# Kernel tuning notes

Hardware: AMD Instinct MI355X
Metric: run time of the kernel (lower is better)

Reference implementation:

```python
import jax, jax.numpy as jnp
import numpy as np

B, T, F, D, H = 16, 512, 32, 256, 256
EPS = 1e-5


def _layernorm(y, g, b):
    m = jnp.mean(y, axis=-1, keepdims=True)
    v = jnp.mean((y - m) ** 2, axis=-1, keepdims=True)
    return (y - m) / jnp.sqrt(v + EPS) * g + b


def setup_inputs() -> dict:
    key = jax.random.key(0)
    ks = jax.random.split(key, 24)
    s = lambda fan_in: 1.0 / np.sqrt(fan_in)
    u = lambda k, shape, fan_in: jax.random.uniform(k, shape, jnp.float32, -s(fan_in), s(fan_in))
    return {
        "x": jax.random.normal(ks[0], (B, T, F), jnp.float32),
        # per-feature Linear(1, D), stacked over F
        "proj_w": u(ks[1], (F, D), 1),
        "proj_b": u(ks[2], (F, D), 1),
        # per-feature scorer GRN(D, H, 1), stacked over F
        "sc_fc1_w": u(ks[3], (F, H, D), D),
        "sc_fc1_b": u(ks[4], (F, H), D),
        "sc_fc2_w": u(ks[5], (F, 1, H), H),
        "sc_fc2_b": u(ks[6], (F, 1), H),
        "sc_gate_w": u(ks[7], (F, 1, 1), 1),
        "sc_gate_b": u(ks[8], (F, 1), 1),
        "sc_skip_w": u(ks[9], (F, 1, D), D),
        "sc_skip_b": u(ks[10], (F, 1), D),
        "sc_ln_g": jnp.ones((F, 1), jnp.float32),
        "sc_ln_b": jnp.zeros((F, 1), jnp.float32),
        # post GRN(D, H, D); in_dim == out_dim -> skip is identity
        "post_fc1_w": u(ks[11], (H, D), D),
        "post_fc1_b": u(ks[12], (H,), D),
        "post_fc2_w": u(ks[13], (D, H), H),
        "post_fc2_b": u(ks[14], (D,), H),
        "post_gate_w": u(ks[15], (D, D), D),
        "post_gate_b": u(ks[16], (D,), D),
        "post_ln_g": jnp.ones((D,), jnp.float32),
        "post_ln_b": jnp.zeros((D,), jnp.float32),
    }


def reference(x, proj_w, proj_b, sc_fc1_w, sc_fc1_b, sc_fc2_w, sc_fc2_b,
              sc_gate_w, sc_gate_b, sc_skip_w, sc_skip_b, sc_ln_g, sc_ln_b,
              post_fc1_w, post_fc1_b, post_fc2_w, post_fc2_b,
              post_gate_w, post_gate_b, post_ln_g, post_ln_b):
    # per-feature embedding: Linear(1 -> D), batched over F
    # E: [B, T, F, D]
    E = x[..., None] * proj_w[None, None] + proj_b[None, None]

    # per-feature scorer GRN(D, H, 1), all F at once
    h = jax.nn.elu(jnp.einsum("btfd,fhd->btfh", E, sc_fc1_w) + sc_fc1_b)
    h = jnp.einsum("btfh,foh->btfo", h, sc_fc2_w) + sc_fc2_b  # [B,T,F,1]
    g = jax.nn.sigmoid(jnp.einsum("btfo,fpo->btfp", h, sc_gate_w) + sc_gate_b)
    skip = jnp.einsum("btfd,fod->btfo", E, sc_skip_w) + sc_skip_b
    y = g * h + (1.0 - g) * skip
    S = _layernorm(y, sc_ln_g, sc_ln_b)  # [B,T,F,1] (last dim size 1)

    # softmax over features, weighted mixture
    W = jax.nn.softmax(S, axis=2)
    mix = jnp.sum(E * W, axis=2)  # [B,T,D]

    # post GRN(D, H, D), skip = identity
    h2 = jax.nn.elu(mix @ post_fc1_w.T + post_fc1_b)
    h2 = h2 @ post_fc2_w.T + post_fc2_b
    g2 = jax.nn.sigmoid(h2 @ post_gate_w.T + post_gate_b)
    y2 = g2 * h2 + (1.0 - g2) * mix
    return _layernorm(y2, post_ln_g, post_ln_b)
```

## Files before the change

### kernel.cpp

```cpp
#include <hip/hip_runtime.h>
#include <hip/hip_bf16.h>
#include <math.h>


typedef __bf16 bf16;
typedef __bf16 bf16x8 __attribute__((ext_vector_type(8)));
typedef __bf16 bf16x4 __attribute__((ext_vector_type(4)));
typedef float f32x4 __attribute__((ext_vector_type(4)));

#define NTOK 8192
#define D_   256
#define F_   32

#define OFF_C      512
#define OFF_WPROJT 2048
#define OFF_FC1    32768
#define OFF_FC2    163840
#define OFF_GATE   294912


__global__ __launch_bounds__(256) void vsn_prep(
    const float* __restrict__ proj_w, const float* __restrict__ proj_b,
    const float* __restrict__ sc_ln_b,
    const float* __restrict__ w1, const float* __restrict__ w2,
    const float* __restrict__ w3,
    float* __restrict__ wsC, bf16* __restrict__ wsWT,
    bf16* __restrict__ o1, bf16* __restrict__ o2, bf16* __restrict__ o3)
{
  const int blk = blockIdx.x;
  if (blk < 24) {
    int g = blk * 256 + threadIdx.x;
    int m = g >> 11;
    int c = g & 2047;
    const float* src = (m == 0) ? w1 : (m == 1) ? w2 : w3;
    bf16* dst = (m == 0) ? o1 : (m == 1) ? o2 : o3;
    int row = c >> 3, ks = c & 7;
    int j = row >> 4, lm = row & 15;
    const float* sp = src + row * 256 + ks * 32;
    bf16* dp = dst + j * 4096 + ks * 512 + lm * 32;
    #pragma unroll
    for (int q = 0; q < 4; q++) {
      float4 a = ((const float4*)sp)[2 * q];
      float4 b = ((const float4*)sp)[2 * q + 1];
      bf16x8 v = {(bf16)a.x, (bf16)a.y, (bf16)a.z, (bf16)a.w,
                  (bf16)b.x, (bf16)b.y, (bf16)b.z, (bf16)b.w};
      *(bf16x8*)(dp + q * 8) = v;
    }
  } else {
    const int d = threadIdx.x;
    float wv[F_];
    float mx = -3.0e38f;
    #pragma unroll
    for (int f = 0; f < F_; f++) { wv[f] = sc_ln_b[f]; mx = fmaxf(mx, wv[f]); }
    float se = 0.0f;
    #pragma unroll
    for (int f = 0; f < F_; f++) { wv[f] = __expf(wv[f] - mx); se += wv[f]; }
    float inv = 1.0f / se;
    float acc = 0.0f;
    #pragma unroll
    for (int f = 0; f < F_; f++) {
      float wf = wv[f] * inv;
      acc += wf * proj_b[f * D_ + d];
      wsWT[d * F_ + f] = (bf16)(wf * proj_w[f * D_ + d]);
    }
    wsC[d] = acc;
  }
}

__global__ __launch_bounds__(256, 2) void vsn_main(
    const float* __restrict__ x,
    const float* __restrict__ wsC,
    const bf16* __restrict__ WT,
    const bf16* __restrict__ FC1, const float* __restrict__ fc1_b,
    const bf16* __restrict__ FC2, const float* __restrict__ fc2_b,
    const bf16* __restrict__ GATE, const float* __restrict__ gate_b,
    const float* __restrict__ ln_g, const float* __restrict__ ln_b,
    float* __restrict__ out)
{
  __shared__ bf16  sAct[2][16][264];
  __shared__ float sLN[4][16][2];

  const int tid  = threadIdx.x;
  const int w    = tid >> 6;
  const int lane = tid & 63;
  const int lm   = lane & 15;
  const int lq   = lane >> 4;
  const int j0   = w * 4;
  const int tok0 = blockIdx.x * 16;

  bf16x4 mixh[4];
  {
    const float* xp = x + (size_t)(tok0 + lm) * F_ + lq * 8;
    float4 x0 = *(const float4*)xp;
    float4 x1 = *(const float4*)(xp + 4);
    bf16x8 a0 = {(bf16)x0.x, (bf16)x0.y, (bf16)x0.z, (bf16)x0.w,
                 (bf16)x1.x, (bf16)x1.y, (bf16)x1.z, (bf16)x1.w};
    #pragma unroll
    for (int jj = 0; jj < 4; jj++) {
      int n = (j0 + jj) * 16 + lm;
      bf16x8 b = *(const bf16x8*)(WT + n * F_ + lq * 8);
      float cv = wsC[n];
      f32x4 acc = {cv, cv, cv, cv};
      acc = __builtin_amdgcn_mfma_f32_16x16x32_bf16(a0, b, acc, 0, 0, 0);
      bf16x4 mh = {(bf16)acc[0], (bf16)acc[1], (bf16)acc[2], (bf16)acc[3]};
      mixh[jj] = mh;
      #pragma unroll
      for (int r = 0; r < 4; r++) sAct[0][lq * 4 + r][n] = mh[r];
    }
  }
  __syncthreads();

  auto gemmPhase = [&](int src, const bf16* __restrict__ W, f32x4* acc) {
    bf16x8 af[8];
    #pragma unroll
    for (int ks = 0; ks < 8; ks++)
      af[ks] = *(const bf16x8*)(&sAct[src][lm][ks * 32 + lq * 8]);
    const bf16* base = W + j0 * 4096 + lm * 32 + lq * 8;
    bf16x8 bb[8];
    #pragma unroll
    for (int ks = 0; ks < 8; ks++)
      bb[ks] = *(const bf16x8*)(base + ks * 512);
    #pragma unroll
    for (int jj = 0; jj < 4; jj++) {
      bf16x8 bn[8];
      if (jj < 3) {
        const bf16* nb = base + (jj + 1) * 4096;
        #pragma unroll
        for (int ks = 0; ks < 8; ks++)
          bn[ks] = *(const bf16x8*)(nb + ks * 512);
      }
      f32x4 a = {0.f, 0.f, 0.f, 0.f};
      acc[jj] = a;
      #pragma unroll
      for (int ks = 0; ks < 8; ks++)
        acc[jj] = __builtin_amdgcn_mfma_f32_16x16x32_bf16(af[ks], bb[ks], acc[jj], 0, 0, 0);
      if (jj < 3) {
        #pragma unroll
        for (int ks = 0; ks < 8; ks++) bb[ks] = bn[ks];
      }
    }
  };

  {
    f32x4 acc[4];
    gemmPhase(0, FC1, acc);
    #pragma unroll
    for (int jj = 0; jj < 4; jj++) {
      int n = (j0 + jj) * 16 + lm;
      float bias = fc1_b[n];
      #pragma unroll
      for (int r = 0; r < 4; r++) {
        float v = acc[jj][r] + bias;
        v = (v > 0.0f) ? v : (__expf(v) - 1.0f);
        sAct[1][lq * 4 + r][n] = (bf16)v;
      }
    }
  }
  __syncthreads();

  bf16x4 h2h[4];
  {
    f32x4 acc[4];
    gemmPhase(1, FC2, acc);
    #pragma unroll
    for (int jj = 0; jj < 4; jj++) {
      int n = (j0 + jj) * 16 + lm;
      float bias = fc2_b[n];
      bf16x4 hh;
      #pragma unroll
      for (int r = 0; r < 4; r++) {
        hh[r] = (bf16)(acc[jj][r] + bias);
        sAct[0][lq * 4 + r][n] = hh[r];
      }
      h2h[jj] = hh;
    }
  }
  __syncthreads();

  f32x4 acc4[4];
  gemmPhase(0, GATE, acc4);
  float rs[4] = {0.f, 0.f, 0.f, 0.f}, rq[4] = {0.f, 0.f, 0.f, 0.f};
  #pragma unroll
  for (int jj = 0; jj < 4; jj++) {
    int n = (j0 + jj) * 16 + lm;
    float bias = gate_b[n];
    #pragma unroll
    for (int r = 0; r < 4; r++) {
      float s = acc4[jj][r] + bias;
      float g = 1.0f / (1.0f + __expf(-s));
      float y = g * (float)h2h[jj][r] + (1.0f - g) * (float)mixh[jj][r];
      acc4[jj][r] = y;
      rs[r] += y;
      rq[r] += y * y;
    }
  }

  #pragma unroll
  for (int r = 0; r < 4; r++) {
    #pragma unroll
    for (int off = 1; off < 16; off <<= 1) {
      rs[r] += __shfl_xor(rs[r], off);
      rq[r] += __shfl_xor(rq[r], off);
    }
  }
  if (lm == 0) {
    #pragma unroll
    for (int r = 0; r < 4; r++) {
      sLN[w][lq * 4 + r][0] = rs[r];
      sLN[w][lq * 4 + r][1] = rq[r];
    }
  }
  __syncthreads();

  const float inv_d = 1.0f / 256.0f;
  float mean[4], rstd[4];
  #pragma unroll
  for (int r = 0; r < 4; r++) {
    int row = lq * 4 + r;
    float S = sLN[0][row][0] + sLN[1][row][0] + sLN[2][row][0] + sLN[3][row][0];
    float Q = sLN[0][row][1] + sLN[1][row][1] + sLN[2][row][1] + sLN[3][row][1];
    float m = S * inv_d;
    mean[r] = m;
    rstd[r] = rsqrtf(Q * inv_d - m * m + 1e-5f);
  }
  #pragma unroll
  for (int jj = 0; jj < 4; jj++) {
    int n = (j0 + jj) * 16 + lm;
    float lg = ln_g[n], lb = ln_b[n];
    #pragma unroll
    for (int r = 0; r < 4; r++) {
      float o = (acc4[jj][r] - mean[r]) * rstd[r] * lg + lb;
      out[(size_t)(tok0 + lq * 4 + r) * D_ + n] = o;
    }
  }
}

extern "C" void kernel_launch(void* const* d_in, const int* in_sizes, int n_in,
                              void* d_out, int out_size, void* d_ws, size_t ws_size,
                              hipStream_t stream) {
  (void)in_sizes; (void)n_in; (void)ws_size; (void)out_size;
  const float* x      = (const float*)d_in[0];
  const float* proj_w = (const float*)d_in[1];
  const float* proj_b = (const float*)d_in[2];
  const float* sclnb  = (const float*)d_in[12];
  const float* fc1w   = (const float*)d_in[13];
  const float* fc1b   = (const float*)d_in[14];
  const float* fc2w   = (const float*)d_in[15];
  const float* fc2b   = (const float*)d_in[16];
  const float* gw     = (const float*)d_in[17];
  const float* gb     = (const float*)d_in[18];
  const float* lng    = (const float*)d_in[19];
  const float* lnb    = (const float*)d_in[20];

  char* ws = (char*)d_ws;
  float* wsC   = (float*)(ws + OFF_C);
  bf16*  wsWT  = (bf16*)(ws + OFF_WPROJT);
  bf16*  bFC1  = (bf16*)(ws + OFF_FC1);
  bf16*  bFC2  = (bf16*)(ws + OFF_FC2);
  bf16*  bGATE = (bf16*)(ws + OFF_GATE);

  vsn_prep<<<25, 256, 0, stream>>>(proj_w, proj_b, sclnb, fc1w, fc2w, gw,
                                   wsC, wsWT, bFC1, bFC2, bGATE);
  vsn_main<<<NTOK / 16, 256, 0, stream>>>(x, wsC, wsWT,
                                          bFC1, fc1b, bFC2, fc2b, bGATE, gb,
                                          lng, lnb, (float*)d_out);
}
```

Before: 121.3 us.

## Fold gate weight into fc2 algebraically and process 32 tokens per block

Precomputes Wgate·Wfc2 and the matching folded bias in the prep kernel, so the gate GEMM reads the fc1 activations directly and runs alongside the fc2 GEMM in one phase. This removes one GEMM stage, one LDS round trip and one barrier. Each block also handles 32 tokens instead of 16, so every loaded weight fragment is reused across two MFMA tiles. The costs are a heavier prep kernel (a serial 256×256×256 fp32 product), more registers per thread with occupancy cut to one block per CU, a grid of only 256 blocks, and a change in bf16 rounding from multiplying the weights ahead of time.

```diff
diff --git a/kernel.cpp b/kernel.cpp
--- a/kernel.cpp
+++ b/kernel.cpp
@@ -13,27 +13,29 @@
 #define F_   32
 
 #define OFF_C      512
-#define OFF_WPROJT 2048
+#define OFF_BP     1536
+#define OFF_WPROJT 4096
 #define OFF_FC1    32768
 #define OFF_FC2    163840
-#define OFF_GATE   294912
+#define OFF_GF     294912
 
 
 __global__ __launch_bounds__(256) void vsn_prep(
     const float* __restrict__ proj_w, const float* __restrict__ proj_b,
     const float* __restrict__ sc_ln_b,
-    const float* __restrict__ w1, const float* __restrict__ w2,
-    const float* __restrict__ w3,
-    float* __restrict__ wsC, bf16* __restrict__ wsWT,
-    bf16* __restrict__ o1, bf16* __restrict__ o2, bf16* __restrict__ o3)
+    const float* __restrict__ fc1w, const float* __restrict__ fc2w,
+    const float* __restrict__ fc2b,
+    const float* __restrict__ gatew, const float* __restrict__ gateb,
+    float* __restrict__ wsC, float* __restrict__ wsBp, bf16* __restrict__ wsWT,
+    bf16* __restrict__ oFC1, bf16* __restrict__ oFC2, bf16* __restrict__ oGF)
 {
   const int blk = blockIdx.x;
-  if (blk < 24) {
+  if (blk < 16) {
     int g = blk * 256 + threadIdx.x;
     int m = g >> 11;
     int c = g & 2047;
-    const float* src = (m == 0) ? w1 : (m == 1) ? w2 : w3;
-    bf16* dst = (m == 0) ? o1 : (m == 1) ? o2 : o3;
+    const float* src = (m == 0) ? fc1w : fc2w;
+    bf16* dst = (m == 0) ? oFC1 : oFC2;
     int row = c >> 3, ks = c & 7;
     int j = row >> 4, lm = row & 15;
     const float* sp = src + row * 256 + ks * 32;
@@ -46,7 +48,7 @@
                   (bf16)b.x, (bf16)b.y, (bf16)b.z, (bf16)b.w};
       *(bf16x8*)(dp + q * 8) = v;
     }
-  } else {
+  } else if (blk == 16) {
     const int d = threadIdx.x;
     float wv[F_];
     float mx = -3.0e38f;
@@ -64,21 +66,48 @@
       wsWT[d * F_ + f] = (bf16)(wf * proj_w[f * D_ + d]);
     }
     wsC[d] = acc;
+  } else {
+    __shared__ float gs[4][257];
+    const int rb = (blk - 17) * 4;
+    const int c = threadIdx.x;
+    #pragma unroll
+    for (int r = 0; r < 4; r++) gs[r][c] = gatew[(rb + r) * 256 + c];
+    __syncthreads();
+    float a0 = 0.f, a1 = 0.f, a2 = 0.f, a3 = 0.f;
+    for (int k = 0; k < 256; k++) {
+      float f = fc2w[k * 256 + c];
+      a0 += gs[0][k] * f;
+      a1 += gs[1][k] * f;
+      a2 += gs[2][k] * f;
+      a3 += gs[3][k] * f;
+    }
+    float accr[4] = {a0, a1, a2, a3};
+    #pragma unroll
+    for (int r = 0; r < 4; r++) {
+      int row = rb + r;
+      oGF[(row >> 4) * 4096 + (c >> 5) * 512 + (row & 15) * 32 + (c & 31)] =
+          (bf16)accr[r];
+    }
+    if (c < 4) {
+      float s = gateb[rb + c];
+      for (int k = 0; k < 256; k++) s += gs[c][k] * fc2b[k];
+      wsBp[rb + c] = s;
+    }
   }
 }
 
-__global__ __launch_bounds__(256, 2) void vsn_main(
+__global__ __launch_bounds__(256, 1) void vsn_main(
     const float* __restrict__ x,
     const float* __restrict__ wsC,
     const bf16* __restrict__ WT,
     const bf16* __restrict__ FC1, const float* __restrict__ fc1_b,
     const bf16* __restrict__ FC2, const float* __restrict__ fc2_b,
-    const bf16* __restrict__ GATE, const float* __restrict__ gate_b,
+    const bf16* __restrict__ GF, const float* __restrict__ bprime,
     const float* __restrict__ ln_g, const float* __restrict__ ln_b,
     float* __restrict__ out)
 {
-  __shared__ bf16  sAct[2][16][264];
-  __shared__ float sLN[4][16][2];
+  __shared__ bf16  sAct[2][32][264];
+  __shared__ float sLN[4][32][2];
 
   const int tid  = threadIdx.x;
   const int w    = tid >> 6;
@@ -86,36 +115,46 @@
   const int lm   = lane & 15;
   const int lq   = lane >> 4;
   const int j0   = w * 4;
-  const int tok0 = blockIdx.x * 16;
-
-  bf16x4 mixh[4];
+  const int tok0 = blockIdx.x * 32;
+
+  bf16x4 mixh[2][4];
   {
-    const float* xp = x + (size_t)(tok0 + lm) * F_ + lq * 8;
-    float4 x0 = *(const float4*)xp;
-    float4 x1 = *(const float4*)(xp + 4);
-    bf16x8 a0 = {(bf16)x0.x, (bf16)x0.y, (bf16)x0.z, (bf16)x0.w,
-                 (bf16)x1.x, (bf16)x1.y, (bf16)x1.z, (bf16)x1.w};
+    bf16x8 a[2];
+    #pragma unroll
+    for (int t = 0; t < 2; t++) {
+      const float* xp = x + (size_t)(tok0 + t * 16 + lm) * F_ + lq * 8;
+      float4 x0 = *(const float4*)xp;
+      float4 x1 = *(const float4*)(xp + 4);
+      bf16x8 av = {(bf16)x0.x, (bf16)x0.y, (bf16)x0.z, (bf16)x0.w,
+                   (bf16)x1.x, (bf16)x1.y, (bf16)x1.z, (bf16)x1.w};
+      a[t] = av;
+    }
     #pragma unroll
     for (int jj = 0; jj < 4; jj++) {
       int n = (j0 + jj) * 16 + lm;
       bf16x8 b = *(const bf16x8*)(WT + n * F_ + lq * 8);
       float cv = wsC[n];
-      f32x4 acc = {cv, cv, cv, cv};
-      acc = __builtin_amdgcn_mfma_f32_16x16x32_bf16(a0, b, acc, 0, 0, 0);
-      bf16x4 mh = {(bf16)acc[0], (bf16)acc[1], (bf16)acc[2], (bf16)acc[3]};
-      mixh[jj] = mh;
-      #pragma unroll
-      for (int r = 0; r < 4; r++) sAct[0][lq * 4 + r][n] = mh[r];
+      #pragma unroll
+      for (int t = 0; t < 2; t++) {
+        f32x4 acc = {cv, cv, cv, cv};
+        acc = __builtin_amdgcn_mfma_f32_16x16x32_bf16(a[t], b, acc, 0, 0, 0);
+        bf16x4 mh = {(bf16)acc[0], (bf16)acc[1], (bf16)acc[2], (bf16)acc[3]};
+        mixh[t][jj] = mh;
+        #pragma unroll
+        for (int r = 0; r < 4; r++) sAct[0][t * 16 + lq * 4 + r][n] = mh[r];
+      }
     }
   }
   __syncthreads();
 
-  auto gemmPhase = [&](int src, const bf16* __restrict__ W, f32x4* acc) {
-    bf16x8 af[8];
-    #pragma unroll
-    for (int ks = 0; ks < 8; ks++)
-      af[ks] = *(const bf16x8*)(&sAct[src][lm][ks * 32 + lq * 8]);
-    const bf16* base = W + j0 * 4096 + lm * 32 + lq * 8;
+  {
+    bf16x8 af[2][8];
+    #pragma unroll
+    for (int t = 0; t < 2; t++)
+      #pragma unroll
+      for (int ks = 0; ks < 8; ks++)
+        af[t][ks] = *(const bf16x8*)(&sAct[0][t * 16 + lm][ks * 32 + lq * 8]);
+    const bf16* base = FC1 + j0 * 4096 + lm * 32 + lq * 8;
     bf16x8 bb[8];
     #pragma unroll
     for (int ks = 0; ks < 8; ks++)
@@ -129,108 +168,121 @@
         for (int ks = 0; ks < 8; ks++)
           bn[ks] = *(const bf16x8*)(nb + ks * 512);
       }
-      f32x4 a = {0.f, 0.f, 0.f, 0.f};
-      acc[jj] = a;
-      #pragma unroll
-      for (int ks = 0; ks < 8; ks++)
-        acc[jj] = __builtin_amdgcn_mfma_f32_16x16x32_bf16(af[ks], bb[ks], acc[jj], 0, 0, 0);
+      f32x4 acc0 = {0.f, 0.f, 0.f, 0.f}, acc1 = {0.f, 0.f, 0.f, 0.f};
+      #pragma unroll
+      for (int ks = 0; ks < 8; ks++) {
+        acc0 = __builtin_amdgcn_mfma_f32_16x16x32_bf16(af[0][ks], bb[ks], acc0, 0, 0, 0);
+        acc1 = __builtin_amdgcn_mfma_f32_16x16x32_bf16(af[1][ks], bb[ks], acc1, 0, 0, 0);
+      }
+      int n = (j0 + jj) * 16 + lm;
+      float bias = fc1_b[n];
+      #pragma unroll
+      for (int r = 0; r < 4; r++) {
+        float v0 = acc0[r] + bias;
+        v0 = (v0 > 0.0f) ? v0 : (__expf(v0) - 1.0f);
+        sAct[1][lq * 4 + r][n] = (bf16)v0;
+        float v1 = acc1[r] + bias;
+        v1 = (v1 > 0.0f) ? v1 : (__expf(v1) - 1.0f);
+        sAct[1][16 + lq * 4 + r][n] = (bf16)v1;
+      }
       if (jj < 3) {
         #pragma unroll
         for (int ks = 0; ks < 8; ks++) bb[ks] = bn[ks];
       }
     }
-  };
-
+  }
+  __syncthreads();
+
+  f32x4 y2[2][4];
   {
-    f32x4 acc[4];
-    gemmPhase(0, FC1, acc);
+    bf16x8 af[2][8];
+    #pragma unroll
+    for (int t = 0; t < 2; t++)
+      #pragma unroll
+      for (int ks = 0; ks < 8; ks++)
+        af[t][ks] = *(const bf16x8*)(&sAct[1][t * 16 + lm][ks * 32 + lq * 8]);
+    const bf16* baseF = FC2 + j0 * 4096 + lm * 32 + lq * 8;
+    const bf16* baseG = GF  + j0 * 4096 + lm * 32 + lq * 8;
+    #pragma unroll
+    for (int jj = 0; jj < 4; jj++) {
+      bf16x8 bF[8], bG[8];
+      #pragma unroll
+      for (int ks = 0; ks < 8; ks++) {
+        bF[ks] = *(const bf16x8*)(baseF + jj * 4096 + ks * 512);
+        bG[ks] = *(const bf16x8*)(baseG + jj * 4096 + ks * 512);
+      }
+      f32x4 hF0 = {0.f,0.f,0.f,0.f}, hF1 = {0.f,0.f,0.f,0.f};
+      f32x4 hG0 = {0.f,0.f,0.f,0.f}, hG1 = {0.f,0.f,0.f,0.f};
+      #pragma unroll
+      for (int ks = 0; ks < 8; ks++) {
+        hF0 = __builtin_amdgcn_mfma_f32_16x16x32_bf16(af[0][ks], bF[ks], hF0, 0, 0, 0);
+        hF1 = __builtin_amdgcn_mfma_f32_16x16x32_bf16(af[1][ks], bF[ks], hF1, 0, 0, 0);
+        hG0 = __builtin_amdgcn_mfma_f32_16x16x32_bf16(af[0][ks], bG[ks], hG0, 0, 0, 0);
+        hG1 = __builtin_amdgcn_mfma_f32_16x16x32_bf16(af[1][ks], bG[ks], hG1, 0, 0, 0);
+      }
+      int n = (j0 + jj) * 16 + lm;
+      float b2v = fc2_b[n];
+      float bpv = bprime[n];
+      #pragma unroll
+      for (int r = 0; r < 4; r++) {
+        float h20 = hF0[r] + b2v;
+        float g0  = 1.0f / (1.0f + __expf(-(hG0[r] + bpv)));
+        y2[0][jj][r] = g0 * h20 + (1.0f - g0) * (float)mixh[0][jj][r];
+        float h21 = hF1[r] + b2v;
+        float g1  = 1.0f / (1.0f + __expf(-(hG1[r] + bpv)));
+        y2[1][jj][r] = g1 * h21 + (1.0f - g1) * (float)mixh[1][jj][r];
+      }
+    }
+  }
+
+  #pragma unroll
+  for (int t = 0; t < 2; t++) {
+    float rs[4] = {0.f,0.f,0.f,0.f}, rq[4] = {0.f,0.f,0.f,0.f};
+    #pragma unroll
+    for (int jj = 0; jj < 4; jj++)
+      #pragma unroll
+      for (int r = 0; r < 4; r++) {
+        float y = y2[t][jj][r];
+        rs[r] += y;
+        rq[r] += y * y;
+      }
+    #pragma unroll
+    for (int r = 0; r < 4; r++) {
+      #pragma unroll
+      for (int off = 1; off < 16; off <<= 1) {
+        rs[r] += __shfl_xor(rs[r], off);
+        rq[r] += __shfl_xor(rq[r], off);
+      }
+      if (lm == 0) {
+        sLN[w][t * 16 + lq * 4 + r][0] = rs[r];
+        sLN[w][t * 16 + lq * 4 + r][1] = rq[r];
+      }
+    }
+  }
+  __syncthreads();
+
+  const float inv_d = 1.0f / 256.0f;
+  #pragma unroll
+  for (int t = 0; t < 2; t++) {
+    float mean[4], rstd[4];
+    #pragma unroll
+    for (int r = 0; r < 4; r++) {
+      int row = t * 16 + lq * 4 + r;
+      float S = sLN[0][row][0] + sLN[1][row][0] + sLN[2][row][0] + sLN[3][row][0];
+      float Q = sLN[0][row][1] + sLN[1][row][1] + sLN[2][row][1] + sLN[3][row][1];
+      float m = S * inv_d;
+      mean[r] = m;
+      rstd[r] = rsqrtf(Q * inv_d - m * m + 1e-5f);
+    }
     #pragma unroll
     for (int jj = 0; jj < 4; jj++) {
       int n = (j0 + jj) * 16 + lm;
-      float bias = fc1_b[n];
+      float lg = ln_g[n], lb = ln_b[n];
       #pragma unroll
       for (int r = 0; r < 4; r++) {
-        float v = acc[jj][r] + bias;
-        v = (v > 0.0f) ? v : (__expf(v) - 1.0f);
-        sAct[1][lq * 4 + r][n] = (bf16)v;
-      }
-    }
-  }
-  __syncthreads();
-
-  bf16x4 h2h[4];
-  {
-    f32x4 acc[4];
-    gemmPhase(1, FC2, acc);
-    #pragma unroll
-    for (int jj = 0; jj < 4; jj++) {
-      int n = (j0 + jj) * 16 + lm;
-      float bias = fc2_b[n];
-      bf16x4 hh;
-      #pragma unroll
-      for (int r = 0; r < 4; r++) {
-        hh[r] = (bf16)(acc[jj][r] + bias);
-        sAct[0][lq * 4 + r][n] = hh[r];
-      }
-      h2h[jj] = hh;
-    }
-  }
-  __syncthreads();
-
-  f32x4 acc4[4];
-  gemmPhase(0, GATE, acc4);
-  float rs[4] = {0.f, 0.f, 0.f, 0.f}, rq[4] = {0.f, 0.f, 0.f, 0.f};
-  #pragma unroll
-  for (int jj = 0; jj < 4; jj++) {
-    int n = (j0 + jj) * 16 + lm;
-    float bias = gate_b[n];
-    #pragma unroll
-    for (int r = 0; r < 4; r++) {
-      float s = acc4[jj][r] + bias;
-      float g = 1.0f / (1.0f + __expf(-s));
-      float y = g * (float)h2h[jj][r] + (1.0f - g) * (float)mixh[jj][r];
-      acc4[jj][r] = y;
-      rs[r] += y;
-      rq[r] += y * y;
-    }
-  }
-
-  #pragma unroll
-  for (int r = 0; r < 4; r++) {
-    #pragma unroll
-    for (int off = 1; off < 16; off <<= 1) {
-      rs[r] += __shfl_xor(rs[r], off);
-      rq[r] += __shfl_xor(rq[r], off);
-    }
-  }
-  if (lm == 0) {
-    #pragma unroll
-    for (int r = 0; r < 4; r++) {
-      sLN[w][lq * 4 + r][0] = rs[r];
-      sLN[w][lq * 4 + r][1] = rq[r];
-    }
-  }
-  __syncthreads();
-
-  const float inv_d = 1.0f / 256.0f;
-  float mean[4], rstd[4];
-  #pragma unroll
-  for (int r = 0; r < 4; r++) {
-    int row = lq * 4 + r;
-    float S = sLN[0][row][0] + sLN[1][row][0] + sLN[2][row][0] + sLN[3][row][0];
-    float Q = sLN[0][row][1] + sLN[1][row][1] + sLN[2][row][1] + sLN[3][row][1];
-    float m = S * inv_d;
-    mean[r] = m;
-    rstd[r] = rsqrtf(Q * inv_d - m * m + 1e-5f);
-  }
-  #pragma unroll
-  for (int jj = 0; jj < 4; jj++) {
-    int n = (j0 + jj) * 16 + lm;
-    float lg = ln_g[n], lb = ln_b[n];
-    #pragma unroll
-    for (int r = 0; r < 4; r++) {
-      float o = (acc4[jj][r] - mean[r]) * rstd[r] * lg + lb;
-      out[(size_t)(tok0 + lq * 4 + r) * D_ + n] = o;
+        float o = (y2[t][jj][r] - mean[r]) * rstd[r] * lg + lb;
+        out[(size_t)(tok0 + t * 16 + lq * 4 + r) * D_ + n] = o;
+      }
     }
   }
 }
@@ -254,14 +306,15 @@
 
   char* ws = (char*)d_ws;
   float* wsC   = (float*)(ws + OFF_C);
+  float* wsBp  = (float*)(ws + OFF_BP);
   bf16*  wsWT  = (bf16*)(ws + OFF_WPROJT);
   bf16*  bFC1  = (bf16*)(ws + OFF_FC1);
   bf16*  bFC2  = (bf16*)(ws + OFF_FC2);
-  bf16*  bGATE = (bf16*)(ws + OFF_GATE);
-
-  vsn_prep<<<25, 256, 0, stream>>>(proj_w, proj_b, sclnb, fc1w, fc2w, gw,
-                                   wsC, wsWT, bFC1, bFC2, bGATE);
-  vsn_main<<<NTOK / 16, 256, 0, stream>>>(x, wsC, wsWT,
-                                          bFC1, fc1b, bFC2, fc2b, bGATE, gb,
+  bf16*  bGF   = (bf16*)(ws + OFF_GF);
+
+  vsn_prep<<<81, 256, 0, stream>>>(proj_w, proj_b, sclnb, fc1w, fc2w, fc2b,
+                                   gw, gb, wsC, wsBp, wsWT, bFC1, bFC2, bGF);
+  vsn_main<<<NTOK / 32, 256, 0, stream>>>(x, wsC, wsWT,
+                                          bFC1, fc1b, bFC2, fc2b, bGF, wsBp,
                                           lng, lnb, (float*)d_out);
 }
```

After: 130.4 us. 1.07x slower.

## Process 32 tokens per block with 8 waves, reusing weight fragments

Applied to the files above, without the earlier changes.

Each block now handles 32 tokens with 512 threads (8 waves), and each wave computes 2 output column tiles for two 16-token row tiles instead of 4 tiles for one. Each B-weight fragment loaded from global memory now feeds two MFMAs, which halves weight traffic per token and gives more independent MFMA chains. The cost is a grid of only 256 blocks, which may underfill a GPU with 256 CUs, plus larger LDS usage and more register pressure per wave.

```diff
diff --git a/kernel.cpp b/kernel.cpp
--- a/kernel.cpp
+++ b/kernel.cpp
@@ -67,7 +67,7 @@
   }
 }
 
-__global__ __launch_bounds__(256, 2) void vsn_main(
+__global__ __launch_bounds__(512, 1) void vsn_main(
     const float* __restrict__ x,
     const float* __restrict__ wsC,
     const bf16* __restrict__ WT,
@@ -77,160 +77,189 @@
     const float* __restrict__ ln_g, const float* __restrict__ ln_b,
     float* __restrict__ out)
 {
-  __shared__ bf16  sAct[2][16][264];
-  __shared__ float sLN[4][16][2];
+  __shared__ bf16  sAct[2][32][264];
+  __shared__ float sLN[8][32][2];
 
   const int tid  = threadIdx.x;
   const int w    = tid >> 6;
   const int lane = tid & 63;
   const int lm   = lane & 15;
   const int lq   = lane >> 4;
-  const int j0   = w * 4;
-  const int tok0 = blockIdx.x * 16;
-
-  bf16x4 mixh[4];
-  {
-    const float* xp = x + (size_t)(tok0 + lm) * F_ + lq * 8;
-    float4 x0 = *(const float4*)xp;
-    float4 x1 = *(const float4*)(xp + 4);
-    bf16x8 a0 = {(bf16)x0.x, (bf16)x0.y, (bf16)x0.z, (bf16)x0.w,
-                 (bf16)x1.x, (bf16)x1.y, (bf16)x1.z, (bf16)x1.w};
-    #pragma unroll
-    for (int jj = 0; jj < 4; jj++) {
+  const int j0   = w * 2;
+  const int tok0 = blockIdx.x * 32;
+
+  bf16x4 mixh[2][2];
+  {
+    bf16x8 a[2];
+    #pragma unroll
+    for (int t = 0; t < 2; t++) {
+      const float* xp = x + (size_t)(tok0 + t * 16 + lm) * F_ + lq * 8;
+      float4 x0 = *(const float4*)xp;
+      float4 x1 = *(const float4*)(xp + 4);
+      bf16x8 av = {(bf16)x0.x, (bf16)x0.y, (bf16)x0.z, (bf16)x0.w,
+                   (bf16)x1.x, (bf16)x1.y, (bf16)x1.z, (bf16)x1.w};
+      a[t] = av;
+    }
+    #pragma unroll
+    for (int jj = 0; jj < 2; jj++) {
       int n = (j0 + jj) * 16 + lm;
       bf16x8 b = *(const bf16x8*)(WT + n * F_ + lq * 8);
       float cv = wsC[n];
-      f32x4 acc = {cv, cv, cv, cv};
-      acc = __builtin_amdgcn_mfma_f32_16x16x32_bf16(a0, b, acc, 0, 0, 0);
-      bf16x4 mh = {(bf16)acc[0], (bf16)acc[1], (bf16)acc[2], (bf16)acc[3]};
-      mixh[jj] = mh;
-      #pragma unroll
-      for (int r = 0; r < 4; r++) sAct[0][lq * 4 + r][n] = mh[r];
-    }
-  }
-  __syncthreads();
-
-  auto gemmPhase = [&](int src, const bf16* __restrict__ W, f32x4* acc) {
-    bf16x8 af[8];
-    #pragma unroll
-    for (int ks = 0; ks < 8; ks++)
-      af[ks] = *(const bf16x8*)(&sAct[src][lm][ks * 32 + lq * 8]);
+      #pragma unroll
+      for (int t = 0; t < 2; t++) {
+        f32x4 acc = {cv, cv, cv, cv};
+        acc = __builtin_amdgcn_mfma_f32_16x16x32_bf16(a[t], b, acc, 0, 0, 0);
+        bf16x4 mh = {(bf16)acc[0], (bf16)acc[1], (bf16)acc[2], (bf16)acc[3]};
+        mixh[t][jj] = mh;
+        #pragma unroll
+        for (int r = 0; r < 4; r++) sAct[0][t * 16 + lq * 4 + r][n] = mh[r];
+      }
+    }
+  }
+  __syncthreads();
+
+  auto gemmPhase = [&](int src, const bf16* __restrict__ W, f32x4 (*acc)[2]) {
+    bf16x8 af[2][8];
+    #pragma unroll
+    for (int t = 0; t < 2; t++)
+      #pragma unroll
+      for (int ks = 0; ks < 8; ks++)
+        af[t][ks] = *(const bf16x8*)(&sAct[src][t * 16 + lm][ks * 32 + lq * 8]);
     const bf16* base = W + j0 * 4096 + lm * 32 + lq * 8;
-    bf16x8 bb[8];
+    bf16x8 bb[8], bn[8];
     #pragma unroll
     for (int ks = 0; ks < 8; ks++)
       bb[ks] = *(const bf16x8*)(base + ks * 512);
     #pragma unroll
-    for (int jj = 0; jj < 4; jj++) {
-      bf16x8 bn[8];
-      if (jj < 3) {
-        const bf16* nb = base + (jj + 1) * 4096;
-        #pragma unroll
-        for (int ks = 0; ks < 8; ks++)
-          bn[ks] = *(const bf16x8*)(nb + ks * 512);
-      }
-      f32x4 a = {0.f, 0.f, 0.f, 0.f};
-      acc[jj] = a;
-      #pragma unroll
-      for (int ks = 0; ks < 8; ks++)
-        acc[jj] = __builtin_amdgcn_mfma_f32_16x16x32_bf16(af[ks], bb[ks], acc[jj], 0, 0, 0);
-      if (jj < 3) {
-        #pragma unroll
-        for (int ks = 0; ks < 8; ks++) bb[ks] = bn[ks];
-      }
+    for (int ks = 0; ks < 8; ks++)
+      bn[ks] = *(const bf16x8*)(base + 4096 + ks * 512);
+    #pragma unroll
+    for (int jj = 0; jj < 2; jj++) {
+      f32x4 a0 = {0.f, 0.f, 0.f, 0.f}, a1 = {0.f, 0.f, 0.f, 0.f};
+      #pragma unroll
+      for (int ks = 0; ks < 8; ks++) {
+        const bf16x8 bv = (jj == 0) ? bb[ks] : bn[ks];
+        a0 = __builtin_amdgcn_mfma_f32_16x16x32_bf16(af[0][ks], bv, a0, 0, 0, 0);
+        a1 = __builtin_amdgcn_mfma_f32_16x16x32_bf16(af[1][ks], bv, a1, 0, 0, 0);
+      }
+      acc[0][jj] = a0;
+      acc[1][jj] = a1;
     }
   };
 
   {
-    f32x4 acc[4];
+    f32x4 acc[2][2];
     gemmPhase(0, FC1, acc);
     #pragma unroll
-    for (int jj = 0; jj < 4; jj++) {
+    for (int jj = 0; jj < 2; jj++) {
       int n = (j0 + jj) * 16 + lm;
       float bias = fc1_b[n];
       #pragma unroll
+      for (int t = 0; t < 2; t++)
+        #pragma unroll
+        for (int r = 0; r < 4; r++) {
+          float v = acc[t][jj][r] + bias;
+          v = (v > 0.0f) ? v : (__expf(v) - 1.0f);
+          sAct[1][t * 16 + lq * 4 + r][n] = (bf16)v;
+        }
+    }
+  }
+  __syncthreads();
+
+  bf16x4 h2h[2][2];
+  {
+    f32x4 acc[2][2];
+    gemmPhase(1, FC2, acc);
+    #pragma unroll
+    for (int jj = 0; jj < 2; jj++) {
+      int n = (j0 + jj) * 16 + lm;
+      float bias = fc2_b[n];
+      #pragma unroll
+      for (int t = 0; t < 2; t++) {
+        bf16x4 hh;
+        #pragma unroll
+        for (int r = 0; r < 4; r++) {
+          hh[r] = (bf16)(acc[t][jj][r] + bias);
+          sAct[0][t * 16 + lq * 4 + r][n] = hh[r];
+        }
+        h2h[t][jj] = hh;
+      }
+    }
+  }
+  __syncthreads();
+
+  f32x4 y2[2][2];
+  {
+    f32x4 acc[2][2];
+    gemmPhase(0, GATE, acc);
+    #pragma unroll
+    for (int jj = 0; jj < 2; jj++) {
+      int n = (j0 + jj) * 16 + lm;
+      float bias = gate_b[n];
+      #pragma unroll
+      for (int t = 0; t < 2; t++)
+        #pragma unroll
+        for (int r = 0; r < 4; r++) {
+          float s = acc[t][jj][r] + bias;
+          float g = 1.0f / (1.0f + __expf(-s));
+          y2[t][jj][r] = g * (float)h2h[t][jj][r] +
+                         (1.0f - g) * (float)mixh[t][jj][r];
+        }
+    }
+  }
+
+  #pragma unroll
+  for (int t = 0; t < 2; t++) {
+    float rs[4] = {0.f, 0.f, 0.f, 0.f}, rq[4] = {0.f, 0.f, 0.f, 0.f};
+    #pragma unroll
+    for (int jj = 0; jj < 2; jj++)
+      #pragma unroll
       for (int r = 0; r < 4; r++) {
-        float v = acc[jj][r] + bias;
-        v = (v > 0.0f) ? v : (__expf(v) - 1.0f);
-        sAct[1][lq * 4 + r][n] = (bf16)v;
-      }
-    }
-  }
-  __syncthreads();
-
-  bf16x4 h2h[4];
-  {
-    f32x4 acc[4];
-    gemmPhase(1, FC2, acc);
-    #pragma unroll
-    for (int jj = 0; jj < 4; jj++) {
-      int n = (j0 + jj) * 16 + lm;
-      float bias = fc2_b[n];
-      bf16x4 hh;
+        float y = y2[t][jj][r];
+        rs[r] += y;
+        rq[r] += y * y;
+      }
+    #pragma unroll
+    for (int r = 0; r < 4; r++) {
+      #pragma unroll
+      for (int off = 1; off < 16; off <<= 1) {
+        rs[r] += __shfl_xor(rs[r], off);
+        rq[r] += __shfl_xor(rq[r], off);
+      }
+      if (lm == 0) {
+        sLN[w][t * 16 + lq * 4 + r][0] = rs[r];
+        sLN[w][t * 16 + lq * 4 + r][1] = rq[r];
+      }
+    }
+  }
+  __syncthreads();
+
+  const float inv_d = 1.0f / 256.0f;
+  #pragma unroll
+  for (int t = 0; t < 2; t++) {
+    float mean[4], rstd[4];
+    #pragma unroll
+    for (int r = 0; r < 4; r++) {
+      int row = t * 16 + lq * 4 + r;
+      float S = 0.f, Q = 0.f;
+      #pragma unroll
+      for (int wv = 0; wv < 8; wv++) {
+        S += sLN[wv][row][0];
+        Q += sLN[wv][row][1];
+      }
+      float m = S * inv_d;
+      mean[r] = m;
+      rstd[r] = rsqrtf(Q * inv_d - m * m + 1e-5f);
+    }
+    #pragma unroll
+    for (int jj = 0; jj < 2; jj++) {
+      int n = (j0 + jj) * 16 + lm;
+      float lg = ln_g[n], lb = ln_b[n];
       #pragma unroll
       for (int r = 0; r < 4; r++) {
-        hh[r] = (bf16)(acc[jj][r] + bias);
-        sAct[0][lq * 4 + r][n] = hh[r];
-      }
-      h2h[jj] = hh;
-    }
-  }
-  __syncthreads();
-
-  f32x4 acc4[4];
-  gemmPhase(0, GATE, acc4);
-  float rs[4] = {0.f, 0.f, 0.f, 0.f}, rq[4] = {0.f, 0.f, 0.f, 0.f};
-  #pragma unroll
-  for (int jj = 0; jj < 4; jj++) {
-    int n = (j0 + jj) * 16 + lm;
-    float bias = gate_b[n];
-    #pragma unroll
-    for (int r = 0; r < 4; r++) {
-      float s = acc4[jj][r] + bias;
-      float g = 1.0f / (1.0f + __expf(-s));
-      float y = g * (float)h2h[jj][r] + (1.0f - g) * (float)mixh[jj][r];
-      acc4[jj][r] = y;
-      rs[r] += y;
-      rq[r] += y * y;
-    }
-  }
-
-  #pragma unroll
-  for (int r = 0; r < 4; r++) {
-    #pragma unroll
-    for (int off = 1; off < 16; off <<= 1) {
-      rs[r] += __shfl_xor(rs[r], off);
-      rq[r] += __shfl_xor(rq[r], off);
-    }
-  }
-  if (lm == 0) {
-    #pragma unroll
-    for (int r = 0; r < 4; r++) {
-      sLN[w][lq * 4 + r][0] = rs[r];
-      sLN[w][lq * 4 + r][1] = rq[r];
-    }
-  }
-  __syncthreads();
-
-  const float inv_d = 1.0f / 256.0f;
-  float mean[4], rstd[4];
-  #pragma unroll
-  for (int r = 0; r < 4; r++) {
-    int row = lq * 4 + r;
-    float S = sLN[0][row][0] + sLN[1][row][0] + sLN[2][row][0] + sLN[3][row][0];
-    float Q = sLN[0][row][1] + sLN[1][row][1] + sLN[2][row][1] + sLN[3][row][1];
-    float m = S * inv_d;
-    mean[r] = m;
-    rstd[r] = rsqrtf(Q * inv_d - m * m + 1e-5f);
-  }
-  #pragma unroll
-  for (int jj = 0; jj < 4; jj++) {
-    int n = (j0 + jj) * 16 + lm;
-    float lg = ln_g[n], lb = ln_b[n];
-    #pragma unroll
-    for (int r = 0; r < 4; r++) {
-      float o = (acc4[jj][r] - mean[r]) * rstd[r] * lg + lb;
-      out[(size_t)(tok0 + lq * 4 + r) * D_ + n] = o;
+        float o = (y2[t][jj][r] - mean[r]) * rstd[r] * lg + lb;
+        out[(size_t)(tok0 + t * 16 + lq * 4 + r) * D_ + n] = o;
+      }
     }
   }
 }
@@ -261,7 +290,7 @@
 
   vsn_prep<<<25, 256, 0, stream>>>(proj_w, proj_b, sclnb, fc1w, fc2w, gw,
                                    wsC, wsWT, bFC1, bFC2, bGATE);
-  vsn_main<<<NTOK / 16, 256, 0, stream>>>(x, wsC, wsWT,
+  vsn_main<<<NTOK / 32, 512, 0, stream>>>(x, wsC, wsWT,
                                           bFC1, fc1b, bFC2, fc2b, bGATE, gb,
                                           lng, lnb, (float*)d_out);
 }
```

After: 115.0 us. -5.2%, faster.
